# Performance work log

Measured on AMD Instinct MI355X. Metric: run time of the kernel, lower is better.

The kernel has to match this reference:

```python
import jax, jax.numpy as jnp
import numpy as np


def setup_inputs() -> dict:
    key = jax.random.key(0)
    k1, k2, k3, k4, k5 = jax.random.split(key, 5)
    B, T_enc, D_enc = 8, 512, 256
    T_dec, D_dec = 256, 512
    encoder_outputs = jax.random.normal(k1, (B, T_enc, D_enc), dtype=jnp.float32)
    decoder_states = jax.random.normal(k2, (B, T_dec, D_dec), dtype=jnp.float32)
    # lecun_uniform-like init: U(-sqrt(3/fan_in), sqrt(3/fan_in))
    lim_e = float(np.sqrt(3.0 / D_enc))
    lim_d = float(np.sqrt(3.0 / D_dec))
    W_enc = jax.random.uniform(k3, (D_enc, D_enc), jnp.float32, -lim_e, lim_e)
    W_dec = jax.random.uniform(k4, (D_dec, D_enc), jnp.float32, -lim_d, lim_d)
    v = jax.random.uniform(k5, (D_enc, 1), jnp.float32, -lim_e, lim_e)
    return {
        "encoder_outputs": encoder_outputs,
        "decoder_states": decoder_states,
        "W_enc": W_enc,
        "W_dec": W_dec,
        "v": v,
    }


def reference(encoder_outputs, decoder_states, W_enc, W_dec, v):
    # Parallel rewrite of the per-timestep keras.backend.rnn loop:
    # every decoder step is independent, so batch all steps at once.
    # encW: (B, T_enc, D_enc), decW: (B, T_dec, D_enc)
    encW = jnp.einsum("bte,ef->btf", encoder_outputs, W_enc)
    decW = jnp.einsum("bsd,df->bsf", decoder_states, W_dec)
    # combined: (B, T_dec, T_enc, D_enc) -- additive attention energies
    combined = jnp.tanh(encW[:, None, :, :] + decW[:, :, None, :])
    alpha = jnp.einsum("bste,e->bst", combined, v[:, 0])  # (B, T_dec, T_enc)
    weights = jax.nn.softmax(alpha, axis=-1)
    # context: (B, T_dec, D_enc) -- attention-weighted sum of encoder frames
    context = jnp.einsum("bst,bte->bse", weights, encoder_outputs)
    return (context, weights)
```

## Files before the change

### kernel.cpp

```cpp
#include <hip/hip_runtime.h>


constexpr int B  = 8;
constexpr int TE = 512;
constexpr int DE = 256;
constexpr int TD = 256;
constexpr int DD = 512;

constexpr float LOG2E  = 1.4426950408889634f;
constexpr float K2     = 2.8853900817779268f;
constexpr float ACLAMP = 10.0f;

typedef float f2 __attribute__((ext_vector_type(2)));

__device__ __forceinline__ float fexp2(float x){ return __builtin_amdgcn_exp2f(x); }
__device__ __forceinline__ float frcp (float x){ return __builtin_amdgcn_rcpf(x); }
__device__ __forceinline__ f2 pk_add(f2 a, f2 b){ f2 d; asm("v_pk_add_f32 %0, %1, %2":"=v"(d):"v"(a),"v"(b)); return d; }
__device__ __forceinline__ f2 pk_mul(f2 a, f2 b){ f2 d; asm("v_pk_mul_f32 %0, %1, %2":"=v"(d):"v"(a),"v"(b)); return d; }
__device__ __forceinline__ f2 pk_fma(f2 a, f2 b, f2 c){ f2 d; asm("v_pk_fma_f32 %0, %1, %2, %3":"=v"(d):"v"(a),"v"(b),"v"(c)); return d; }

__device__ __forceinline__ float e2z(float z){
  return fexp2(K2 * fminf(fmaxf(z, -ACLAMP), ACLAMP));
}

__global__ __launch_bounds__(256)
void prep_kernel(const float* __restrict__ enc, const float* __restrict__ Wenc,
                 const float* __restrict__ dec, const float* __restrict__ Wdec,
                 float* __restrict__ encE, float* __restrict__ decE)
{
  __shared__ __align__(16) float LT[16][257];
  const int tid = threadIdx.x;
  const int bid = blockIdx.x;
  if (bid < 256){
    const int r0 = bid*16;
    const int b = r0 >> 9, t0 = r0 & (TE-1);
    const int col = tid;
    float acc[16];
    #pragma unroll
    for (int r=0;r<16;r++) acc[r]=0.f;
    const float* Arow = enc + (size_t)r0*DE;
    const float* wp   = Wenc + col;
    for (int k4=0;k4<DE/4;k4++){
      const float w0 = wp[(size_t)(4*k4  )*DE];
      const float w1 = wp[(size_t)(4*k4+1)*DE];
      const float w2 = wp[(size_t)(4*k4+2)*DE];
      const float w3 = wp[(size_t)(4*k4+3)*DE];
      #pragma unroll
      for (int r=0;r<16;r++){
        const float4 av = *(const float4*)(Arow + (size_t)r*DE + 4*k4);
        acc[r] += av.x*w0 + av.y*w1 + av.z*w2 + av.w*w3;
      }
    }
    #pragma unroll
    for (int r=0;r<16;r++) LT[r][col] = e2z(acc[r]);
    __syncthreads();
    const int wv = tid>>6, lane = tid&63, le = lane>>2, jj = lane&3;
    #pragma unroll
    for (int p=0;p<4;p++){
      const int e = p*64 + wv*16 + le;
      float4 val;
      val.x = LT[4*jj+0][e]; val.y = LT[4*jj+1][e];
      val.z = LT[4*jj+2][e]; val.w = LT[4*jj+3][e];
      *(float4*)(encE + (size_t)(b*DE + e)*TE + t0 + 4*jj) = val;
    }
  } else {
    const int r0 = (bid-256)*8;
    const int col = tid;
    float acc[8];
    #pragma unroll
    for (int r=0;r<8;r++) acc[r]=0.f;
    const float* Arow = dec + (size_t)r0*DD;
    const float* wp   = Wdec + col;
    for (int k4=0;k4<DD/4;k4++){
      const float w0 = wp[(size_t)(4*k4  )*DE];
      const float w1 = wp[(size_t)(4*k4+1)*DE];
      const float w2 = wp[(size_t)(4*k4+2)*DE];
      const float w3 = wp[(size_t)(4*k4+3)*DE];
      #pragma unroll
      for (int r=0;r<8;r++){
        const float4 av = *(const float4*)(Arow + (size_t)r*DD + 4*k4);
        acc[r] += av.x*w0 + av.y*w1 + av.z*w2 + av.w*w3;
      }
    }
    #pragma unroll
    for (int r=0;r<8;r++)
      decE[(size_t)(r0+r)*DE + col] = e2z(acc[r]);
  }
}

template<bool USE_DWT>
__global__ __launch_bounds__(1024, 8)
void attn_kernel(const float* __restrict__ enc, const float* __restrict__ dec,
                 const float* __restrict__ Wdec, const float* __restrict__ v,
                 const float* __restrict__ encE, const float* __restrict__ decE,
                 float* __restrict__ outCtx, float* __restrict__ outW)
{
  __shared__ __align__(16) float ebp[DE*4*2];
  __shared__ __align__(16) float vnp[DE*2];
  __shared__ __align__(16) float part[16*TE];
  __shared__ float wsum[16], rs[4];

  const int tid = threadIdx.x;
  const int bid = ((blockIdx.x & 7) << 6) | (blockIdx.x >> 3);
  const int b  = bid >> 6;
  const int s0 = (bid & 63)*4;

  if (USE_DWT){
    if (tid < DE){
      const float* dp = decE + (size_t)(b*TD + s0)*DE + tid;
      const float g0 = dp[0], g1 = dp[DE], g2 = dp[2*DE], g3 = dp[3*DE];
      float4 q0; q0.x=g0; q0.y=g0; q0.z=g1; q0.w=g1;
      float4 q1; q1.x=g2; q1.y=g2; q1.z=g3; q1.w=g3;
      *(float4*)&ebp[tid*8]   = q0;
      *(float4*)&ebp[tid*8+4] = q1;
      const float vnv = -2.f*LOG2E*v[tid];
      *(f2*)&vnp[tid*2] = f2{vnv, vnv};
    }
    __syncthreads();
  } else {
    {
      const float* src = dec + (size_t)(b*TD + s0)*DD;
      part[tid] = src[tid];
      part[tid + 1024] = src[tid + 1024];
    }
    __syncthreads();
    const int s = tid >> 8, e = tid & 255;
    float a = 0.f;
    const float* wp  = Wdec + e;
    const float* dsp = part + s*DD;
    #pragma unroll 2
    for (int k4=0;k4<DD/4;k4++){
      const float4 qd = *(const float4*)(dsp + 4*k4);
      a += qd.x*wp[(size_t)(4*k4  )*DE] + qd.y*wp[(size_t)(4*k4+1)*DE]
         + qd.z*wp[(size_t)(4*k4+2)*DE] + qd.w*wp[(size_t)(4*k4+3)*DE];
    }
    const float eb = e2z(a);
    __syncthreads();
    *(f2*)&ebp[(e*4 + s)*2] = f2{eb, eb};
    if (s == 0) *(f2*)&vnp[e*2] = f2{-2.f*LOG2E*v[e], -2.f*LOG2E*v[e]};
    __syncthreads();
  }

  {
    const int g = tid >> 8, q = tid & 255;
    f2 acc0 = f2{0.f,0.f}, acc1 = f2{0.f,0.f}, acc2 = f2{0.f,0.f}, acc3 = f2{0.f,0.f};
    const f2 one2 = {1.f, 1.f};
    const float* xp = encE + (size_t)(b*DE + 64*g)*TE + 2*q;
    const float* ep = ebp + 64*g*8;
    const float* np = vnp + 64*g*2;
    #pragma unroll 2
    for (int i=0;i<64;i++){
      const f2 ea = *(const f2*)(xp + (size_t)i*TE);
      const float4 e01 = *(const float4*)(ep + i*8);
      const float4 e23 = *(const float4*)(ep + i*8 + 4);
      const f2 vn2 = *(const f2*)(np + i*2);
      const f2 d0 = pk_add(one2, pk_mul(ea, f2{e01.x, e01.y}));
      const f2 d1 = pk_add(one2, pk_mul(ea, f2{e01.z, e01.w}));
      const f2 d2 = pk_add(one2, pk_mul(ea, f2{e23.x, e23.y}));
      const f2 d3 = pk_add(one2, pk_mul(ea, f2{e23.z, e23.w}));
      const f2 D01 = pk_mul(d0, d1);
      const f2 D23 = pk_mul(d2, d3);
      const f2 R01 = {frcp(D01.x), frcp(D01.y)};
      const f2 R23 = {frcp(D23.x), frcp(D23.y)};
      acc0 = pk_fma(vn2, pk_mul(R01, d1), acc0);
      acc1 = pk_fma(vn2, pk_mul(R01, d0), acc1);
      acc2 = pk_fma(vn2, pk_mul(R23, d3), acc2);
      acc3 = pk_fma(vn2, pk_mul(R23, d2), acc3);
    }
    *(f2*)&part[(g*4 + 0)*TE + 2*q] = acc0;
    *(f2*)&part[(g*4 + 1)*TE + 2*q] = acc1;
    *(f2*)&part[(g*4 + 2)*TE + 2*q] = acc2;
    *(f2*)&part[(g*4 + 3)*TE + 2*q] = acc3;
  }
  __syncthreads();

  {
    const int w = tid >> 6, lane = tid & 63;
    const int s = w >> 2, c = w & 3;
    const int t0 = c*128 + 2*lane;
    f2 a = f2{0.f,0.f};
    #pragma unroll
    for (int g=0; g<4; g++){
      const f2 p = *(const f2*)&part[(g*4 + s)*TE + t0];
      a.x += p.x; a.y += p.y;
    }
    f2 ex; ex.x = fexp2(a.x); ex.y = fexp2(a.y);
    *(f2*)&part[(0*4 + s)*TE + t0] = ex;
    float sum = ex.x + ex.y;
    #pragma unroll
    for (int off=32; off>=1; off>>=1) sum += __shfl_xor(sum, off);
    if (lane==0) wsum[w] = sum;
    __syncthreads();
    const float S = wsum[s*4] + wsum[s*4+1] + wsum[s*4+2] + wsum[s*4+3];
    const float r = 1.0f / S;
    f2 wo; wo.x = ex.x*r; wo.y = ex.y*r;
    *(f2*)(outW + (size_t)(b*TD + s0 + s)*TE + t0) = wo;
    if (lane==0 && c==0) rs[s] = r;
  }

  {
    const int h = tid >> 8, e = tid & 255;
    float c0=0.f, c1=0.f, c2=0.f, c3=0.f;
    const float* encB = enc + (size_t)(b*TE + 128*h)*DE + e;
    const int tb = 128*h;
    #pragma unroll 2
    for (int t4=0;t4<32;t4++){
      const float4 q0 = *(const float4*)&part[0*TE + tb + 4*t4];
      const float4 q1 = *(const float4*)&part[1*TE + tb + 4*t4];
      const float4 q2 = *(const float4*)&part[2*TE + tb + 4*t4];
      const float4 q3 = *(const float4*)&part[3*TE + tb + 4*t4];
      const float f0 = encB[(size_t)(4*t4  )*DE];
      const float f1 = encB[(size_t)(4*t4+1)*DE];
      const float f2_ = encB[(size_t)(4*t4+2)*DE];
      const float f3 = encB[(size_t)(4*t4+3)*DE];
      c0 += q0.x*f0+q0.y*f1+q0.z*f2_+q0.w*f3;
      c1 += q1.x*f0+q1.y*f1+q1.z*f2_+q1.w*f3;
      c2 += q2.x*f0+q2.y*f1+q2.z*f2_+q2.w*f3;
      c3 += q3.x*f0+q3.y*f1+q3.z*f2_+q3.w*f3;
    }
    float* partc = part + 8*TE;
    partc[(h*4+0)*DE + e] = c0;
    partc[(h*4+1)*DE + e] = c1;
    partc[(h*4+2)*DE + e] = c2;
    partc[(h*4+3)*DE + e] = c3;
  }
  __syncthreads();
  if (tid < DE){
    const float* partc = part + 8*TE;
    #pragma unroll
    for (int s=0;s<4;s++){
      const float val = (partc[(0*4+s)*DE + tid] + partc[(1*4+s)*DE + tid]
                       + partc[(2*4+s)*DE + tid] + partc[(3*4+s)*DE + tid]) * rs[s];
      outCtx[(size_t)(b*TD + s0 + s)*DE + tid] = val;
    }
  }
}

extern "C" void kernel_launch(void* const* d_in, const int* in_sizes, int n_in,
                              void* d_out, int out_size, void* d_ws, size_t ws_size,
                              hipStream_t stream)
{
  const float* enc  = (const float*)d_in[0];
  const float* dec  = (const float*)d_in[1];
  const float* Wenc = (const float*)d_in[2];
  const float* Wdec = (const float*)d_in[3];
  const float* v    = (const float*)d_in[4];
  float* outCtx = (float*)d_out;
  float* outW   = outCtx + (size_t)B*TD*DE;
  float* encE   = (float*)d_ws;
  float* decE   = encE + (size_t)B*DE*TE;

  const bool use_dwt = ws_size >= (size_t)(B*DE*TE + B*TD*DE)*sizeof(float);

  hipLaunchKernelGGL(prep_kernel, dim3(512), dim3(256), 0, stream,
                     enc, Wenc, dec, Wdec, encE, decE);
  if (use_dwt){
    hipLaunchKernelGGL((attn_kernel<true>), dim3(512), dim3(1024), 0, stream,
                       enc, dec, Wdec, v, encE, decE, outCtx, outW);
  } else {
    hipLaunchKernelGGL((attn_kernel<false>), dim3(512), dim3(1024), 0, stream,
                       enc, dec, Wdec, v, encE, decE, outCtx, outW);
  }
}
```

Before: 79.90 us.

## Halve decoder steps per attention block, use 512-thread blocks and fused packed FMA

The attention kernel now handles 2 decoder steps per block with 512 threads over 1024 blocks, instead of 4 steps with 1024 threads over 512 blocks. The prep kernel likewise uses smaller row tiles over twice as many blocks. The energy loop now loads float4 encoder terms and uses packed FMA in place of separate packed mul and add. Softmax probabilities go to a separate LDS buffer. The aim is better occupancy and scheduling flexibility, at the cost of reading each batch's encE tile twice as often, which adds L2 traffic and lowers reuse.

```diff
diff --git a/kernel.cpp b/kernel.cpp
--- a/kernel.cpp
+++ b/kernel.cpp
@@ -15,7 +15,6 @@
 
 __device__ __forceinline__ float fexp2(float x){ return __builtin_amdgcn_exp2f(x); }
 __device__ __forceinline__ float frcp (float x){ return __builtin_amdgcn_rcpf(x); }
-__device__ __forceinline__ f2 pk_add(f2 a, f2 b){ f2 d; asm("v_pk_add_f32 %0, %1, %2":"=v"(d):"v"(a),"v"(b)); return d; }
 __device__ __forceinline__ f2 pk_mul(f2 a, f2 b){ f2 d; asm("v_pk_mul_f32 %0, %1, %2":"=v"(d):"v"(a),"v"(b)); return d; }
 __device__ __forceinline__ f2 pk_fma(f2 a, f2 b, f2 c){ f2 d; asm("v_pk_fma_f32 %0, %1, %2, %3":"=v"(d):"v"(a),"v"(b),"v"(c)); return d; }
 
@@ -28,16 +27,16 @@
                  const float* __restrict__ dec, const float* __restrict__ Wdec,
                  float* __restrict__ encE, float* __restrict__ decE)
 {
-  __shared__ __align__(16) float LT[16][257];
+  __shared__ __align__(16) float LT[8][260];
   const int tid = threadIdx.x;
   const int bid = blockIdx.x;
-  if (bid < 256){
-    const int r0 = bid*16;
+  if (bid < 512){
+    const int r0 = bid*8;
     const int b = r0 >> 9, t0 = r0 & (TE-1);
     const int col = tid;
-    float acc[16];
-    #pragma unroll
-    for (int r=0;r<16;r++) acc[r]=0.f;
+    float acc[8];
+    #pragma unroll
+    for (int r=0;r<8;r++) acc[r]=0.f;
     const float* Arow = enc + (size_t)r0*DE;
     const float* wp   = Wenc + col;
     for (int k4=0;k4<DE/4;k4++){
@@ -46,29 +45,29 @@
       const float w2 = wp[(size_t)(4*k4+2)*DE];
       const float w3 = wp[(size_t)(4*k4+3)*DE];
       #pragma unroll
-      for (int r=0;r<16;r++){
+      for (int r=0;r<8;r++){
         const float4 av = *(const float4*)(Arow + (size_t)r*DE + 4*k4);
         acc[r] += av.x*w0 + av.y*w1 + av.z*w2 + av.w*w3;
       }
     }
     #pragma unroll
-    for (int r=0;r<16;r++) LT[r][col] = e2z(acc[r]);
-    __syncthreads();
-    const int wv = tid>>6, lane = tid&63, le = lane>>2, jj = lane&3;
-    #pragma unroll
-    for (int p=0;p<4;p++){
-      const int e = p*64 + wv*16 + le;
+    for (int r=0;r<8;r++) LT[r][col] = e2z(acc[r]);
+    __syncthreads();
+    const int wv = tid>>6, lane = tid&63, le = lane>>1, jj = lane&1;
+    #pragma unroll
+    for (int p=0;p<2;p++){
+      const int e = p*128 + wv*32 + le;
       float4 val;
       val.x = LT[4*jj+0][e]; val.y = LT[4*jj+1][e];
       val.z = LT[4*jj+2][e]; val.w = LT[4*jj+3][e];
       *(float4*)(encE + (size_t)(b*DE + e)*TE + t0 + 4*jj) = val;
     }
   } else {
-    const int r0 = (bid-256)*8;
+    const int r0 = (bid-512)*4;
     const int col = tid;
-    float acc[8];
-    #pragma unroll
-    for (int r=0;r<8;r++) acc[r]=0.f;
+    float acc[4];
+    #pragma unroll
+    for (int r=0;r<4;r++) acc[r]=0.f;
     const float* Arow = dec + (size_t)r0*DD;
     const float* wp   = Wdec + col;
     for (int k4=0;k4<DD/4;k4++){
@@ -77,51 +76,50 @@
       const float w2 = wp[(size_t)(4*k4+2)*DE];
       const float w3 = wp[(size_t)(4*k4+3)*DE];
       #pragma unroll
-      for (int r=0;r<8;r++){
+      for (int r=0;r<4;r++){
         const float4 av = *(const float4*)(Arow + (size_t)r*DD + 4*k4);
         acc[r] += av.x*w0 + av.y*w1 + av.z*w2 + av.w*w3;
       }
     }
     #pragma unroll
-    for (int r=0;r<8;r++)
+    for (int r=0;r<4;r++)
       decE[(size_t)(r0+r)*DE + col] = e2z(acc[r]);
   }
 }
 
 template<bool USE_DWT>
-__global__ __launch_bounds__(1024, 8)
+__global__ __launch_bounds__(512, 8)
 void attn_kernel(const float* __restrict__ enc, const float* __restrict__ dec,
                  const float* __restrict__ Wdec, const float* __restrict__ v,
                  const float* __restrict__ encE, const float* __restrict__ decE,
                  float* __restrict__ outCtx, float* __restrict__ outW)
 {
-  __shared__ __align__(16) float ebp[DE*4*2];
+  __shared__ __align__(16) float ebp[DE*4];
   __shared__ __align__(16) float vnp[DE*2];
-  __shared__ __align__(16) float part[16*TE];
-  __shared__ float wsum[16], rs[4];
+  __shared__ __align__(16) float part[8*TE];
+  __shared__ __align__(16) float pl[2*TE];
+  __shared__ float wsum[8], rs[2];
 
   const int tid = threadIdx.x;
-  const int bid = ((blockIdx.x & 7) << 6) | (blockIdx.x >> 3);
-  const int b  = bid >> 6;
-  const int s0 = (bid & 63)*4;
+  const int bid = ((blockIdx.x & 7) << 7) | (blockIdx.x >> 3);
+  const int b   = bid >> 7;
+  const int sp0 = (bid & 127)*2;
 
   if (USE_DWT){
     if (tid < DE){
-      const float* dp = decE + (size_t)(b*TD + s0)*DE + tid;
-      const float g0 = dp[0], g1 = dp[DE], g2 = dp[2*DE], g3 = dp[3*DE];
-      float4 q0; q0.x=g0; q0.y=g0; q0.z=g1; q0.w=g1;
-      float4 q1; q1.x=g2; q1.y=g2; q1.z=g3; q1.w=g3;
-      *(float4*)&ebp[tid*8]   = q0;
-      *(float4*)&ebp[tid*8+4] = q1;
+      const float* dp = decE + (size_t)(b*TD + sp0)*DE + tid;
+      const float g0 = dp[0], g1 = dp[DE];
+      float4 q; q.x = g0; q.y = g0; q.z = g1; q.w = g1;
+      *(float4*)&ebp[tid*4] = q;
       const float vnv = -2.f*LOG2E*v[tid];
       *(f2*)&vnp[tid*2] = f2{vnv, vnv};
     }
     __syncthreads();
   } else {
     {
-      const float* src = dec + (size_t)(b*TD + s0)*DD;
+      const float* src = dec + (size_t)(b*TD + sp0)*DD;
       part[tid] = src[tid];
-      part[tid + 1024] = src[tid + 1024];
+      part[tid + 512] = src[tid + 512];
     }
     __syncthreads();
     const int s = tid >> 8, e = tid & 255;
@@ -136,41 +134,42 @@
     }
     const float eb = e2z(a);
     __syncthreads();
-    *(f2*)&ebp[(e*4 + s)*2] = f2{eb, eb};
+    *(f2*)&ebp[e*4 + 2*s] = f2{eb, eb};
     if (s == 0) *(f2*)&vnp[e*2] = f2{-2.f*LOG2E*v[e], -2.f*LOG2E*v[e]};
     __syncthreads();
   }
 
   {
-    const int g = tid >> 8, q = tid & 255;
-    f2 acc0 = f2{0.f,0.f}, acc1 = f2{0.f,0.f}, acc2 = f2{0.f,0.f}, acc3 = f2{0.f,0.f};
+    const int g = tid >> 7, q = tid & 127;
+    f2 acc0L = f2{0.f,0.f}, acc0H = f2{0.f,0.f};
+    f2 acc1L = f2{0.f,0.f}, acc1H = f2{0.f,0.f};
     const f2 one2 = {1.f, 1.f};
-    const float* xp = encE + (size_t)(b*DE + 64*g)*TE + 2*q;
-    const float* ep = ebp + 64*g*8;
+    const float* xp = encE + (size_t)(b*DE + 64*g)*TE + 4*q;
+    const float* ep = ebp + 64*g*4;
     const float* np = vnp + 64*g*2;
     #pragma unroll 2
     for (int i=0;i<64;i++){
-      const f2 ea = *(const f2*)(xp + (size_t)i*TE);
-      const float4 e01 = *(const float4*)(ep + i*8);
-      const float4 e23 = *(const float4*)(ep + i*8 + 4);
-      const f2 vn2 = *(const f2*)(np + i*2);
-      const f2 d0 = pk_add(one2, pk_mul(ea, f2{e01.x, e01.y}));
-      const f2 d1 = pk_add(one2, pk_mul(ea, f2{e01.z, e01.w}));
-      const f2 d2 = pk_add(one2, pk_mul(ea, f2{e23.x, e23.y}));
-      const f2 d3 = pk_add(one2, pk_mul(ea, f2{e23.z, e23.w}));
-      const f2 D01 = pk_mul(d0, d1);
-      const f2 D23 = pk_mul(d2, d3);
-      const f2 R01 = {frcp(D01.x), frcp(D01.y)};
-      const f2 R23 = {frcp(D23.x), frcp(D23.y)};
-      acc0 = pk_fma(vn2, pk_mul(R01, d1), acc0);
-      acc1 = pk_fma(vn2, pk_mul(R01, d0), acc1);
-      acc2 = pk_fma(vn2, pk_mul(R23, d3), acc2);
-      acc3 = pk_fma(vn2, pk_mul(R23, d2), acc3);
-    }
-    *(f2*)&part[(g*4 + 0)*TE + 2*q] = acc0;
-    *(f2*)&part[(g*4 + 1)*TE + 2*q] = acc1;
-    *(f2*)&part[(g*4 + 2)*TE + 2*q] = acc2;
-    *(f2*)&part[(g*4 + 3)*TE + 2*q] = acc3;
+      const float4 ea = *(const float4*)(xp + (size_t)i*TE);
+      const float4 eb = *(const float4*)(ep + i*4);
+      const f2 vn2    = *(const f2*)(np + i*2);
+      const f2 taL = {ea.x, ea.y}, taH = {ea.z, ea.w};
+      const f2 d0L = pk_fma(taL, f2{eb.x, eb.y}, one2);
+      const f2 d0H = pk_fma(taH, f2{eb.x, eb.y}, one2);
+      const f2 d1L = pk_fma(taL, f2{eb.z, eb.w}, one2);
+      const f2 d1H = pk_fma(taH, f2{eb.z, eb.w}, one2);
+      const f2 DL = pk_mul(d0L, d1L);
+      const f2 DH = pk_mul(d0H, d1H);
+      const f2 RL = {frcp(DL.x), frcp(DL.y)};
+      const f2 RH = {frcp(DH.x), frcp(DH.y)};
+      acc0L = pk_fma(vn2, pk_mul(RL, d1L), acc0L);
+      acc0H = pk_fma(vn2, pk_mul(RH, d1H), acc0H);
+      acc1L = pk_fma(vn2, pk_mul(RL, d0L), acc1L);
+      acc1H = pk_fma(vn2, pk_mul(RH, d0H), acc1H);
+    }
+    float4 st0; st0.x=acc0L.x; st0.y=acc0L.y; st0.z=acc0H.x; st0.w=acc0H.y;
+    float4 st1; st1.x=acc1L.x; st1.y=acc1L.y; st1.z=acc1H.x; st1.w=acc1H.y;
+    *(float4*)&part[(g*2 + 0)*TE + 4*q] = st0;
+    *(float4*)&part[(g*2 + 1)*TE + 4*q] = st1;
   }
   __syncthreads();
 
@@ -181,11 +180,11 @@
     f2 a = f2{0.f,0.f};
     #pragma unroll
     for (int g=0; g<4; g++){
-      const f2 p = *(const f2*)&part[(g*4 + s)*TE + t0];
+      const f2 p = *(const f2*)&part[(g*2 + s)*TE + t0];
       a.x += p.x; a.y += p.y;
     }
     f2 ex; ex.x = fexp2(a.x); ex.y = fexp2(a.y);
-    *(f2*)&part[(0*4 + s)*TE + t0] = ex;
+    *(f2*)&pl[s*TE + t0] = ex;
     float sum = ex.x + ex.y;
     #pragma unroll
     for (int off=32; off>=1; off>>=1) sum += __shfl_xor(sum, off);
@@ -194,45 +193,35 @@
     const float S = wsum[s*4] + wsum[s*4+1] + wsum[s*4+2] + wsum[s*4+3];
     const float r = 1.0f / S;
     f2 wo; wo.x = ex.x*r; wo.y = ex.y*r;
-    *(f2*)(outW + (size_t)(b*TD + s0 + s)*TE + t0) = wo;
+    *(f2*)(outW + (size_t)(b*TD + sp0 + s)*TE + t0) = wo;
     if (lane==0 && c==0) rs[s] = r;
   }
 
   {
     const int h = tid >> 8, e = tid & 255;
-    float c0=0.f, c1=0.f, c2=0.f, c3=0.f;
-    const float* encB = enc + (size_t)(b*TE + 128*h)*DE + e;
-    const int tb = 128*h;
+    float c0=0.f, c1=0.f;
+    const float* encB = enc + (size_t)(b*TE + 256*h)*DE + e;
+    const float* pb = pl + 256*h;
     #pragma unroll 2
-    for (int t4=0;t4<32;t4++){
-      const float4 q0 = *(const float4*)&part[0*TE + tb + 4*t4];
-      const float4 q1 = *(const float4*)&part[1*TE + tb + 4*t4];
-      const float4 q2 = *(const float4*)&part[2*TE + tb + 4*t4];
-      const float4 q3 = *(const float4*)&part[3*TE + tb + 4*t4];
+    for (int t4=0;t4<64;t4++){
+      const float4 q0 = *(const float4*)(pb + 0*TE + 4*t4);
+      const float4 q1 = *(const float4*)(pb + 1*TE + 4*t4);
       const float f0 = encB[(size_t)(4*t4  )*DE];
       const float f1 = encB[(size_t)(4*t4+1)*DE];
       const float f2_ = encB[(size_t)(4*t4+2)*DE];
       const float f3 = encB[(size_t)(4*t4+3)*DE];
       c0 += q0.x*f0+q0.y*f1+q0.z*f2_+q0.w*f3;
       c1 += q1.x*f0+q1.y*f1+q1.z*f2_+q1.w*f3;
-      c2 += q2.x*f0+q2.y*f1+q2.z*f2_+q2.w*f3;
-      c3 += q3.x*f0+q3.y*f1+q3.z*f2_+q3.w*f3;
-    }
-    float* partc = part + 8*TE;
-    partc[(h*4+0)*DE + e] = c0;
-    partc[(h*4+1)*DE + e] = c1;
-    partc[(h*4+2)*DE + e] = c2;
-    partc[(h*4+3)*DE + e] = c3;
+    }
+    float* partc = part;
+    partc[(h*2+0)*DE + e] = c0;
+    partc[(h*2+1)*DE + e] = c1;
   }
   __syncthreads();
-  if (tid < DE){
-    const float* partc = part + 8*TE;
-    #pragma unroll
-    for (int s=0;s<4;s++){
-      const float val = (partc[(0*4+s)*DE + tid] + partc[(1*4+s)*DE + tid]
-                       + partc[(2*4+s)*DE + tid] + partc[(3*4+s)*DE + tid]) * rs[s];
-      outCtx[(size_t)(b*TD + s0 + s)*DE + tid] = val;
-    }
+  {
+    const int sp = tid >> 8, e = tid & 255;
+    const float val = (part[(0*2+sp)*DE + e] + part[(1*2+sp)*DE + e]) * rs[sp];
+    outCtx[(size_t)(b*TD + sp0 + sp)*DE + e] = val;
   }
 }
 
@@ -252,13 +241,13 @@
 
   const bool use_dwt = ws_size >= (size_t)(B*DE*TE + B*TD*DE)*sizeof(float);
 
-  hipLaunchKernelGGL(prep_kernel, dim3(512), dim3(256), 0, stream,
-                     enc, Wenc, dec, Wdec, encE, decE);
+  hipLaunchKernelGGL(prep_kernel, dim3(use_dwt ? 1024 : 512), dim3(256), 0,
+                     stream, enc, Wenc, dec, Wdec, encE, decE);
   if (use_dwt){
-    hipLaunchKernelGGL((attn_kernel<true>), dim3(512), dim3(1024), 0, stream,
+    hipLaunchKernelGGL((attn_kernel<true>), dim3(1024), dim3(512), 0, stream,
                        enc, dec, Wdec, v, encE, decE, outCtx, outW);
   } else {
-    hipLaunchKernelGGL((attn_kernel<false>), dim3(512), dim3(1024), 0, stream,
+    hipLaunchKernelGGL((attn_kernel<false>), dim3(1024), dim3(512), 0, stream,
                        enc, dec, Wdec, v, encE, decE, outCtx, outW);
   }
 }
```

Result: slower. 87.13 us (+9.1%).
